# Kernel optimization log

Measured on AMD Instinct MI355X. Metric: run time of the kernel, lower is better.

## Reference

```python
import jax, jax.numpy as jnp
import numpy as np

N = 50000      # nodes
E = 800000     # edges
CIN = 128
CH = 128
COUT = 64
EPS = 1e-5     # BatchNorm eps


def setup_inputs() -> dict:
    key = jax.random.key(0)
    ks = jax.random.split(key, 16)
    s = 0.1  # weight scale for numerical stability
    return {
        "x": jax.random.normal(ks[0], (N, CIN), jnp.float32),
        "edge_index": jax.random.randint(ks[1], (2, E), 0, N, jnp.int32),
        "edge_weights": jax.random.uniform(ks[2], (E,), jnp.float32),
        "w1": jax.random.normal(ks[3], (CIN, CH), jnp.float32) * s,
        "b1": jnp.zeros((CH,), jnp.float32),
        "bn1_g": jnp.ones((CH,), jnp.float32),
        "bn1_b": jnp.zeros((CH,), jnp.float32),
        "bn1_m": jax.random.normal(ks[4], (CH,), jnp.float32) * 0.1,
        "bn1_v": jax.random.uniform(ks[5], (CH,), jnp.float32) + 0.5,
        "conv_ws": jax.random.normal(ks[6], (2, CH, CH), jnp.float32) * s,
        "conv_bs": jnp.zeros((2, CH), jnp.float32),
        "bns_g": jnp.ones((2, CH), jnp.float32),
        "bns_b": jnp.zeros((2, CH), jnp.float32),
        "bns_m": jax.random.normal(ks[7], (2, CH), jnp.float32) * 0.1,
        "bns_v": jax.random.uniform(ks[8], (2, CH), jnp.float32) + 0.5,
        "lin1_w": jax.random.normal(ks[9], (CH, CH), jnp.float32) * s,
        "lin1_b": jnp.zeros((CH,), jnp.float32),
        "lin2_w": jax.random.normal(ks[10], (CH, COUT), jnp.float32) * s,
        "lin2_b": jnp.zeros((COUT,), jnp.float32),
    }


def _bn(h, g, b, m, v):
    # BatchNorm1d in eval mode: running statistics
    return (h - m) * jax.lax.rsqrt(v + EPS) * g + b


def _gcn(h, w, b, src, dst, norm, n):
    # GCNConv: out[dst] += norm_e * (h @ W)[src]  (self loops already in src/dst)
    h = h @ w
    msg = h[src] * norm[:, None]                 # [E+N, CH]
    return jax.ops.segment_sum(msg, dst, num_segments=n) + b


def reference(x, edge_index, edge_weights, w1, b1, bn1_g, bn1_b, bn1_m, bn1_v,
              conv_ws, conv_bs, bns_g, bns_b, bns_m, bns_v,
              lin1_w, lin1_b, lin2_w, lin2_b):
    n = x.shape[0]
    loop = jnp.arange(n, dtype=edge_index.dtype)
    src = jnp.concatenate([edge_index[0], loop])
    dst = jnp.concatenate([edge_index[1], loop])
    ew = jnp.concatenate([edge_weights, jnp.ones((n,), edge_weights.dtype)])
    # symmetric degree normalization (PyG gcn_norm)
    deg = jax.ops.segment_sum(ew, dst, num_segments=n)
    dis = jnp.where(deg > 0, jax.lax.rsqrt(deg), 0.0)
    norm = dis[src] * ew * dis[dst]

    lrelu = jax.nn.leaky_relu  # slope 0.01, matches F.leaky_relu default
    h = lrelu(_bn(_gcn(x, w1, b1, src, dst, norm, n), bn1_g, bn1_b, bn1_m, bn1_v))
    for i in range(conv_ws.shape[0]):
        h = lrelu(_bn(_gcn(h, conv_ws[i], conv_bs[i], src, dst, norm, n),
                      bns_g[i], bns_b[i], bns_m[i], bns_v[i]) + h)
    h = lrelu(h @ lin1_w + lin1_b)
    # dropout is identity in eval mode
    return h @ lin2_w + lin2_b
```

## Files before the change

kernel.cpp:

```cpp
#include <hip/hip_runtime.h>
#include <hip/hip_bf16.h>


constexpr int   NN    = 50000;
constexpr int   EE    = 800000;
constexpr int   CH    = 128;
constexpr int   SLOTS = 64;
constexpr int   NBUK  = 782;
constexpr int   RCAP  = 2048;
constexpr int   EPB   = 4096;
constexpr float EPS   = 1e-5f;

typedef __attribute__((ext_vector_type(8))) short bf16x8;
typedef __attribute__((ext_vector_type(4))) float f32x4;
typedef unsigned long long u64;
typedef unsigned short u16;

__device__ inline u16 f2bf_rne(float f) {
  unsigned u = __float_as_uint(f);
  unsigned r = u + 0x7fffu + ((u >> 16) & 1u);
  return (u16)(r >> 16);
}
__device__ inline float bf2f(unsigned h16) {
  return __uint_as_float(h16 << 16);
}


__global__ __launch_bounds__(256) void bin_kernel(const int* __restrict__ ei,
                                                  const float* __restrict__ ew,
                                                  unsigned* __restrict__ gcur,
                                                  u64* __restrict__ bins) {
  __shared__ unsigned cnt[NBUK];
  __shared__ unsigned base[NBUK];
  const int tid = threadIdx.x;
  for (int b = tid; b < NBUK; b += 256) cnt[b] = 0;
  __syncthreads();
  const int e0 = blockIdx.x * EPB;
  unsigned pk[16]; u16 bkt[16]; u16 rnk[16]; unsigned char dl[16];
  #pragma unroll
  for (int i = 0; i < 16; i++) {
    int e = e0 + i * 256 + tid;
    if (e < EE) {
      int s = ei[e], d = ei[EE + e];
      float w = ew[e];
      bkt[i] = (u16)(d >> 6);
      dl[i]  = (unsigned char)(d & 63);
      pk[i]  = ((unsigned)f2bf_rne(w) << 16) | (unsigned)s;
      rnk[i] = (u16)atomicAdd(&cnt[bkt[i]], 1u);
    } else bkt[i] = 0xffffu;
  }
  __syncthreads();
  for (int b = tid; b < NBUK; b += 256) {
    unsigned c = cnt[b];
    base[b] = c ? atomicAdd(&gcur[b * 16], c) : 0u;
  }
  __syncthreads();
  #pragma unroll
  for (int i = 0; i < 16; i++) {
    if (bkt[i] == 0xffffu) continue;
    unsigned pos = base[bkt[i]] + rnk[i];
    if (pos < RCAP)
      bins[(size_t)bkt[i] * RCAP + pos] = ((u64)dl[i] << 32) | pk[i];
  }
}


__global__ __launch_bounds__(256) void scatter_kernel(const unsigned* __restrict__ gcur,
                                                      const u64* __restrict__ bins,
                                                      unsigned* __restrict__ ell,
                                                      float* __restrict__ dis) {
  __shared__ unsigned rank[64];
  __shared__ float    wsum[64];
  const int b   = blockIdx.x;
  const int tid = threadIdx.x;
  if (tid < 64) { rank[tid] = 1u; wsum[tid] = 0.f; }
  __syncthreads();
  unsigned cnt = gcur[b * 16];
  if (cnt > RCAP) cnt = RCAP;
  const u64* src = bins + (size_t)b * RCAP;
  for (unsigned i = tid; i < cnt; i += 256) {
    u64 v = src[i];
    unsigned pk = (unsigned)v;
    unsigned dl = (unsigned)(v >> 32);
    unsigned r = atomicAdd(&rank[dl], 1u);
    if (r < SLOTS)
      ell[((size_t)(b * 64 + dl)) * SLOTS + r] = pk;
    atomicAdd(&wsum[dl], bf2f(pk >> 16));
  }
  __syncthreads();
  if (tid < 64) {
    int node = b * 64 + tid;
    if (node < NN) {
      unsigned c = rank[tid];
      if (c > SLOTS) c = SLOTS;
      ell[(size_t)node * SLOTS] = c;
      dis[node] = rsqrtf(1.0f + wsum[tid]);
    }
  }
}

constexpr int NB_WZ = (73728 + 384 + 255) / 256;

__global__ void wswz_kernel(
    const float* __restrict__ w1, const float* __restrict__ bn1_g, const float* __restrict__ bn1_v,
    const float* __restrict__ conv_ws, const float* __restrict__ bns_g, const float* __restrict__ bns_v,
    const float* __restrict__ lin1_w, const float* __restrict__ lin2_w,
    const float* __restrict__ b1, const float* __restrict__ bn1_b, const float* __restrict__ bn1_m,
    const float* __restrict__ conv_bs, const float* __restrict__ bns_b, const float* __restrict__ bns_m,
    u16* __restrict__ w1h, u16* __restrict__ w1l,
    u16* __restrict__ c0h, u16* __restrict__ c0l,
    u16* __restrict__ c1h, u16* __restrict__ c1l,
    u16* __restrict__ l1h, u16* __restrict__ l1l,
    u16* __restrict__ l2h, u16* __restrict__ l2l,
    float* __restrict__ beff)
{
  int idx = blockIdx.x * 256 + threadIdx.x;
  if (idx >= 73728) {
    int r = idx - 73728;
    if (r >= 384) return;
    int l = r >> 7, c = r & 127;
    float bc, gg, bb, mm, vv;
    if (l == 0) { bc = b1[c]; gg = bn1_g[c]; bb = bn1_b[c]; mm = bn1_m[c]; vv = bn1_v[c]; }
    else {
      int o = (l - 1) * 128 + c;
      bc = conv_bs[o]; gg = bns_g[o]; bb = bns_b[o]; mm = bns_m[o]; vv = bns_v[o];
    }
    beff[r] = (bc - mm) * gg * rsqrtf(vv + EPS) + bb;
    return;
  }
  const float* W; const float* g = nullptr; const float* v = nullptr;
  u16 *hi, *lo; int CO = 128; int local;
  if      (idx < 16384) { W = w1;              g = bn1_g;     v = bn1_v;     hi = w1h; lo = w1l; local = idx; }
  else if (idx < 32768) { W = conv_ws;         g = bns_g;     v = bns_v;     hi = c0h; lo = c0l; local = idx - 16384; }
  else if (idx < 49152) { W = conv_ws + 16384; g = bns_g+128; v = bns_v+128; hi = c1h; lo = c1l; local = idx - 32768; }
  else if (idx < 65536) { W = lin1_w;                                        hi = l1h; lo = l1l; local = idx - 49152; }
  else                  { W = lin2_w;                                        hi = l2h; lo = l2l; local = idx - 65536; CO = 64; }
  int k = local / CO, n = local % CO;
  float w = W[local];
  if (g) w *= g[n] * rsqrtf(v[n] + EPS);
  int NCT = CO / 16;
  int kchunk = k >> 5, kin = k & 31, quad = kin >> 3, j = kin & 7;
  int ct = n >> 4, l = (quad << 4) | (n & 15);
  size_t pos = ((size_t)(kchunk * NCT + ct) * 64 + l) * 8 + j;
  u16 h = f2bf_rne(w);
  hi[pos] = h;
  lo[pos] = f2bf_rne(w - bf2f(h));
}

__global__ __launch_bounds__(256) void gemm1_kernel(
    const float* __restrict__ Ain,
    const u16* __restrict__ Whi, const u16* __restrict__ Wlo,
    const float* __restrict__ dis, u16* __restrict__ Cout)
{
  __shared__ float lds[64][CH + 4];
  const int tid  = threadIdx.x;
  const int wave = tid >> 6;
  const int lane = tid & 63;
  const int quad = lane >> 4;
  const int mrow = lane & 15;
  const int row0 = blockIdx.x * 64;

  int arow = row0 + wave * 16 + mrow;
  if (arow >= NN) arow = NN - 1;

  bf16x8 ahi[4], alo[4];
  const float* Ar = Ain + (size_t)arow * CH;
  #pragma unroll
  for (int c = 0; c < 4; c++) {
    int off = c * 32 + quad * 8;
    float4 f0 = *(const float4*)(Ar + off);
    float4 f1 = *(const float4*)(Ar + off + 4);
    float f[8] = {f0.x, f0.y, f0.z, f0.w, f1.x, f1.y, f1.z, f1.w};
    #pragma unroll
    for (int j = 0; j < 8; j++) {
      u16 h = f2bf_rne(f[j]);
      ahi[c][j] = (short)h;
      alo[c][j] = (short)f2bf_rne(f[j] - bf2f(h));
    }
  }

  f32x4 acc[8];
  #pragma unroll
  for (int t = 0; t < 8; t++) acc[t] = (f32x4){0.f, 0.f, 0.f, 0.f};
  #pragma unroll
  for (int c = 0; c < 4; c++) {
    #pragma unroll
    for (int t = 0; t < 8; t++) {
      size_t base = ((size_t)(c * 8 + t) * 64 + lane) * 8;
      bf16x8 bh = *(const bf16x8*)(Whi + base);
      bf16x8 bl = *(const bf16x8*)(Wlo + base);
      acc[t] = __builtin_amdgcn_mfma_f32_16x16x32_bf16(ahi[c], bh, acc[t], 0, 0, 0);
      acc[t] = __builtin_amdgcn_mfma_f32_16x16x32_bf16(alo[c], bh, acc[t], 0, 0, 0);
      acc[t] = __builtin_amdgcn_mfma_f32_16x16x32_bf16(ahi[c], bl, acc[t], 0, 0, 0);
    }
  }

  #pragma unroll
  for (int t = 0; t < 8; t++)
    #pragma unroll
    for (int r = 0; r < 4; r++)
      lds[wave * 16 + quad * 4 + r][t * 16 + mrow] = acc[t][r];
  __syncthreads();

  #pragma unroll
  for (int i = tid; i < 64 * CH / 4; i += 256) {
    int row = (i * 4) / CH;
    int col = (i * 4) % CH;
    int grow = row0 + row;
    if (grow >= NN) continue;
    float rs = dis[grow];
    const float* lp = &lds[row][col];
    u16* cp = (u16*)Cout + (size_t)grow * CH + col;
    unsigned p0 = ((unsigned)f2bf_rne(lp[1] * rs) << 16) | f2bf_rne(lp[0] * rs);
    unsigned p1 = ((unsigned)f2bf_rne(lp[3] * rs) << 16) | f2bf_rne(lp[2] * rs);
    *(uint2*)cp = make_uint2(p0, p1);
  }
}

template<bool RES>
__global__ __launch_bounds__(256, 6) void fuse_kernel(
    const u16* __restrict__ hwin,
    const unsigned* __restrict__ ell, const float* __restrict__ dis,
    const float* __restrict__ beff, const u16* __restrict__ res,
    const u16* __restrict__ Whi, const u16* __restrict__ Wlo,
    u16* __restrict__ hout, u16* __restrict__ hwout)
{
  __shared__ unsigned hs[16][68];
  const int tid  = threadIdx.x;
  const int wave = tid >> 6;
  const int lane = tid & 63;
  const int sub  = lane & 15;
  const int grp  = lane >> 4;
  const int row0 = blockIdx.x * 16;

  const int nbase = row0 + wave * 4;
  {
    int nd0 = nbase < NN ? nbase : NN - 1;
    unsigned wcur = ell[(size_t)nd0 * SLOTS + lane];
    for (int r = 0; r < 4; r++) {
      int node = nbase + r;
      int nd = node < NN ? node : NN - 1;
      unsigned myword = wcur;
      if (r < 3) {
        int n2 = node + 1 < NN ? node + 1 : NN - 1;
        wcur = ell[(size_t)n2 * SLOTS + lane];
      }
      int cnt = __shfl((int)myword, 0);
      if (cnt > SLOTS) cnt = SLOTS;
      float a[8] = {0.f, 0.f, 0.f, 0.f, 0.f, 0.f, 0.f, 0.f};
      for (int j = 0; j < cnt; j += 16) {
        unsigned sidx[4]; float wv[4];
        #pragma unroll
        for (int q = 0; q < 4; q++) {
          int jj = j + q * 4 + grp;
          unsigned e = (unsigned)__shfl((int)myword, jj & 63);
          float    w = (jj == 0) ? 1.0f : bf2f(e >> 16);
          unsigned s = (jj == 0) ? (unsigned)nd : (e & 0xffffu);
          if (jj >= cnt) { w = 0.f; s = (unsigned)nd; }
          sidx[q] = s; wv[q] = w;
        }
        uint4 h[4];
        #pragma unroll
        for (int q = 0; q < 4; q++)
          h[q] = *(const uint4*)(hwin + (size_t)sidx[q] * CH + sub * 8);
        #pragma unroll
        for (int q = 0; q < 4; q++) {
          float w = wv[q];
          a[0] = fmaf(w, bf2f(h[q].x & 0xffffu), a[0]); a[1] = fmaf(w, bf2f(h[q].x >> 16), a[1]);
          a[2] = fmaf(w, bf2f(h[q].y & 0xffffu), a[2]); a[3] = fmaf(w, bf2f(h[q].y >> 16), a[3]);
          a[4] = fmaf(w, bf2f(h[q].z & 0xffffu), a[4]); a[5] = fmaf(w, bf2f(h[q].z >> 16), a[5]);
          a[6] = fmaf(w, bf2f(h[q].w & 0xffffu), a[6]); a[7] = fmaf(w, bf2f(h[q].w >> 16), a[7]);
        }
      }
      #pragma unroll
      for (int k = 0; k < 8; k++) {
        a[k] += __shfl_xor(a[k], 16);
        a[k] += __shfl_xor(a[k], 32);
      }
      if (grp == 0) {
        float disd = dis[nd];
        int c = sub * 8;
        float4 be0 = *(const float4*)(beff + c);
        float4 be1 = *(const float4*)(beff + c + 4);
        float y[8];
        y[0] = a[0] * disd + be0.x; y[1] = a[1] * disd + be0.y;
        y[2] = a[2] * disd + be0.z; y[3] = a[3] * disd + be0.w;
        y[4] = a[4] * disd + be1.x; y[5] = a[5] * disd + be1.y;
        y[6] = a[6] * disd + be1.z; y[7] = a[7] * disd + be1.w;
        if constexpr (RES) {
          uint4 rr = *(const uint4*)(res + (size_t)nd * CH + c);
          y[0] += bf2f(rr.x & 0xffffu); y[1] += bf2f(rr.x >> 16);
          y[2] += bf2f(rr.y & 0xffffu); y[3] += bf2f(rr.y >> 16);
          y[4] += bf2f(rr.z & 0xffffu); y[5] += bf2f(rr.z >> 16);
          y[6] += bf2f(rr.w & 0xffffu); y[7] += bf2f(rr.w >> 16);
        }
        #pragma unroll
        for (int k = 0; k < 8; k++) y[k] = y[k] > 0.f ? y[k] : 0.01f * y[k];
        uint4 o;
        o.x = ((unsigned)f2bf_rne(y[1]) << 16) | f2bf_rne(y[0]);
        o.y = ((unsigned)f2bf_rne(y[3]) << 16) | f2bf_rne(y[2]);
        o.z = ((unsigned)f2bf_rne(y[5]) << 16) | f2bf_rne(y[4]);
        o.w = ((unsigned)f2bf_rne(y[7]) << 16) | f2bf_rne(y[6]);
        if (node < NN) *(uint4*)(hout + (size_t)node * CH + c) = o;
        *(uint4*)&hs[wave * 4 + r][sub * 4] = o;
      }
    }
  }
  __syncthreads();

  bf16x8 af[4];
  #pragma unroll
  for (int c = 0; c < 4; c++)
    af[c] = *(const bf16x8*)&hs[sub][c * 16 + grp * 4];

  f32x4 acc[2];
  #pragma unroll
  for (int t = 0; t < 2; t++) acc[t] = (f32x4){0.f, 0.f, 0.f, 0.f};
  #pragma unroll
  for (int c = 0; c < 4; c++) {
    #pragma unroll
    for (int t = 0; t < 2; t++) {
      size_t base = ((size_t)(c * 8 + wave * 2 + t) * 64 + lane) * 8;
      bf16x8 bh = *(const bf16x8*)(Whi + base);
      bf16x8 bl = *(const bf16x8*)(Wlo + base);
      acc[t] = __builtin_amdgcn_mfma_f32_16x16x32_bf16(af[c], bh, acc[t], 0, 0, 0);
      acc[t] = __builtin_amdgcn_mfma_f32_16x16x32_bf16(af[c], bl, acc[t], 0, 0, 0);
    }
  }

  #pragma unroll
  for (int r = 0; r < 4; r++) {
    int grow = row0 + grp * 4 + r;
    if (grow >= NN) continue;
    float rs = dis[grow];
    #pragma unroll
    for (int t = 0; t < 2; t++)
      hwout[(size_t)grow * CH + wave * 32 + t * 16 + sub] = f2bf_rne(acc[t][r] * rs);
  }
}

__global__ __launch_bounds__(256, 6) void fuse_last_kernel(
    const u16* __restrict__ hwin,
    const unsigned* __restrict__ ell, const float* __restrict__ dis,
    const float* __restrict__ beff, const u16* __restrict__ res,
    const u16* __restrict__ l1h, const u16* __restrict__ l1l,
    const float* __restrict__ b1,
    const u16* __restrict__ l2h, const u16* __restrict__ l2l,
    const float* __restrict__ b2, float* __restrict__ out)
{
  __shared__ unsigned hs[16][68];
  __shared__ float    fs[16][132];
  const int tid  = threadIdx.x;
  const int wave = tid >> 6;
  const int lane = tid & 63;
  const int sub  = lane & 15;
  const int grp  = lane >> 4;
  const int row0 = blockIdx.x * 16;

  const int nbase = row0 + wave * 4;
  {
    int nd0 = nbase < NN ? nbase : NN - 1;
    unsigned wcur = ell[(size_t)nd0 * SLOTS + lane];
    for (int r = 0; r < 4; r++) {
      int node = nbase + r;
      int nd = node < NN ? node : NN - 1;
      unsigned myword = wcur;
      if (r < 3) {
        int n2 = node + 1 < NN ? node + 1 : NN - 1;
        wcur = ell[(size_t)n2 * SLOTS + lane];
      }
      int cnt = __shfl((int)myword, 0);
      if (cnt > SLOTS) cnt = SLOTS;
      float a[8] = {0.f, 0.f, 0.f, 0.f, 0.f, 0.f, 0.f, 0.f};
      for (int j = 0; j < cnt; j += 16) {
        unsigned sidx[4]; float wv[4];
        #pragma unroll
        for (int q = 0; q < 4; q++) {
          int jj = j + q * 4 + grp;
          unsigned e = (unsigned)__shfl((int)myword, jj & 63);
          float    w = (jj == 0) ? 1.0f : bf2f(e >> 16);
          unsigned s = (jj == 0) ? (unsigned)nd : (e & 0xffffu);
          if (jj >= cnt) { w = 0.f; s = (unsigned)nd; }
          sidx[q] = s; wv[q] = w;
        }
        uint4 h[4];
        #pragma unroll
        for (int q = 0; q < 4; q++)
          h[q] = *(const uint4*)(hwin + (size_t)sidx[q] * CH + sub * 8);
        #pragma unroll
        for (int q = 0; q < 4; q++) {
          float w = wv[q];
          a[0] = fmaf(w, bf2f(h[q].x & 0xffffu), a[0]); a[1] = fmaf(w, bf2f(h[q].x >> 16), a[1]);
          a[2] = fmaf(w, bf2f(h[q].y & 0xffffu), a[2]); a[3] = fmaf(w, bf2f(h[q].y >> 16), a[3]);
          a[4] = fmaf(w, bf2f(h[q].z & 0xffffu), a[4]); a[5] = fmaf(w, bf2f(h[q].z >> 16), a[5]);
          a[6] = fmaf(w, bf2f(h[q].w & 0xffffu), a[6]); a[7] = fmaf(w, bf2f(h[q].w >> 16), a[7]);
        }
      }
      #pragma unroll
      for (int k = 0; k < 8; k++) {
        a[k] += __shfl_xor(a[k], 16);
        a[k] += __shfl_xor(a[k], 32);
      }
      if (grp == 0) {
        float disd = dis[nd];
        int c = sub * 8;
        float4 be0 = *(const float4*)(beff + c);
        float4 be1 = *(const float4*)(beff + c + 4);
        float y[8];
        y[0] = a[0] * disd + be0.x; y[1] = a[1] * disd + be0.y;
        y[2] = a[2] * disd + be0.z; y[3] = a[3] * disd + be0.w;
        y[4] = a[4] * disd + be1.x; y[5] = a[5] * disd + be1.y;
        y[6] = a[6] * disd + be1.z; y[7] = a[7] * disd + be1.w;
        uint4 rr = *(const uint4*)(res + (size_t)nd * CH + c);
        y[0] += bf2f(rr.x & 0xffffu); y[1] += bf2f(rr.x >> 16);
        y[2] += bf2f(rr.y & 0xffffu); y[3] += bf2f(rr.y >> 16);
        y[4] += bf2f(rr.z & 0xffffu); y[5] += bf2f(rr.z >> 16);
        y[6] += bf2f(rr.w & 0xffffu); y[7] += bf2f(rr.w >> 16);
        #pragma unroll
        for (int k = 0; k < 8; k++) y[k] = y[k] > 0.f ? y[k] : 0.01f * y[k];
        uint4 o;
        o.x = ((unsigned)f2bf_rne(y[1]) << 16) | f2bf_rne(y[0]);
        o.y = ((unsigned)f2bf_rne(y[3]) << 16) | f2bf_rne(y[2]);
        o.z = ((unsigned)f2bf_rne(y[5]) << 16) | f2bf_rne(y[4]);
        o.w = ((unsigned)f2bf_rne(y[7]) << 16) | f2bf_rne(y[6]);
        *(uint4*)&hs[wave * 4 + r][sub * 4] = o;
      }
    }
  }
  __syncthreads();

  bf16x8 af[4];
  #pragma unroll
  for (int c = 0; c < 4; c++)
    af[c] = *(const bf16x8*)&hs[sub][c * 16 + grp * 4];

  f32x4 acc[2];
  #pragma unroll
  for (int t = 0; t < 2; t++) acc[t] = (f32x4){0.f, 0.f, 0.f, 0.f};
  #pragma unroll
  for (int c = 0; c < 4; c++) {
    #pragma unroll
    for (int t = 0; t < 2; t++) {
      size_t base = ((size_t)(c * 8 + wave * 2 + t) * 64 + lane) * 8;
      bf16x8 bh = *(const bf16x8*)(l1h + base);
      bf16x8 bl = *(const bf16x8*)(l1l + base);
      acc[t] = __builtin_amdgcn_mfma_f32_16x16x32_bf16(af[c], bh, acc[t], 0, 0, 0);
      acc[t] = __builtin_amdgcn_mfma_f32_16x16x32_bf16(af[c], bl, acc[t], 0, 0, 0);
    }
  }
  #pragma unroll
  for (int t = 0; t < 2; t++) {
    int col = wave * 32 + t * 16 + sub;
    float bb = b1[col];
    #pragma unroll
    for (int r = 0; r < 4; r++) {
      float x = acc[t][r] + bb;
      x = x > 0.f ? x : 0.01f * x;
      fs[grp * 4 + r][col] = x;
    }
  }
  __syncthreads();

  f32x4 acc2 = (f32x4){0.f, 0.f, 0.f, 0.f};
  #pragma unroll
  for (int c = 0; c < 4; c++) {
    bf16x8 ahi, alo;
    const float* lp = &fs[sub][c * 32 + grp * 8];
    float4 f0 = *(const float4*)lp;
    float4 f1 = *(const float4*)(lp + 4);
    float f[8] = {f0.x, f0.y, f0.z, f0.w, f1.x, f1.y, f1.z, f1.w};
    #pragma unroll
    for (int j = 0; j < 8; j++) {
      u16 h = f2bf_rne(f[j]);
      ahi[j] = (short)h;
      alo[j] = (short)f2bf_rne(f[j] - bf2f(h));
    }
    size_t base = ((size_t)(c * 4 + wave) * 64 + lane) * 8;
    bf16x8 bh = *(const bf16x8*)(l2h + base);
    bf16x8 bl = *(const bf16x8*)(l2l + base);
    acc2 = __builtin_amdgcn_mfma_f32_16x16x32_bf16(ahi, bh, acc2, 0, 0, 0);
    acc2 = __builtin_amdgcn_mfma_f32_16x16x32_bf16(alo, bh, acc2, 0, 0, 0);
    acc2 = __builtin_amdgcn_mfma_f32_16x16x32_bf16(ahi, bl, acc2, 0, 0, 0);
  }
  {
    float bb = b2[wave * 16 + sub];
    #pragma unroll
    for (int r = 0; r < 4; r++) {
      int grow = row0 + grp * 4 + r;
      if (grow < NN)
        out[(size_t)grow * 64 + wave * 16 + sub] = acc2[r] + bb;
    }
  }
}


extern "C" void kernel_launch(void* const* d_in, const int* in_sizes, int n_in,
                              void* d_out, int out_size, void* d_ws, size_t ws_size,
                              hipStream_t stream) {
  const float* x       = (const float*)d_in[0];
  const int*   ei      = (const int*)  d_in[1];
  const float* ew      = (const float*)d_in[2];
  const float* w1      = (const float*)d_in[3];
  const float* b1      = (const float*)d_in[4];
  const float* bn1_g   = (const float*)d_in[5];
  const float* bn1_b   = (const float*)d_in[6];
  const float* bn1_m   = (const float*)d_in[7];
  const float* bn1_v   = (const float*)d_in[8];
  const float* conv_ws = (const float*)d_in[9];
  const float* conv_bs = (const float*)d_in[10];
  const float* bns_g   = (const float*)d_in[11];
  const float* bns_b   = (const float*)d_in[12];
  const float* bns_m   = (const float*)d_in[13];
  const float* bns_v   = (const float*)d_in[14];
  const float* lin1_w  = (const float*)d_in[15];
  const float* lin1_b  = (const float*)d_in[16];
  const float* lin2_w  = (const float*)d_in[17];
  const float* lin2_b  = (const float*)d_in[18];
  float* out = (float*)d_out;

  size_t off = 0;
  auto alloc = [&](size_t elems) -> void* {
    void* p = (char*)d_ws + off * 4;
    off += (elems + 3) & ~(size_t)3;
    return p;
  };
  unsigned* gcur = (unsigned*)alloc(NBUK * 16);
  u64*      bins = (u64*)     alloc((size_t)NBUK * RCAP * 2);
  unsigned* ell  = (unsigned*)alloc((size_t)NN * SLOTS);
  float*    dis  = (float*)   alloc(NN);
  float*    beff = (float*)   alloc(3 * CH);
  u16*      hwa  = (u16*)     alloc((size_t)NN * CH / 2);
  u16*      hwb  = (u16*)     alloc((size_t)NN * CH / 2);
  u16*      h1   = (u16*)     alloc((size_t)NN * CH / 2);
  u16*      h2   = (u16*)     alloc((size_t)NN * CH / 2);
  u16* w1h = (u16*)alloc(CH * CH / 2); u16* w1l = (u16*)alloc(CH * CH / 2);
  u16* c0h = (u16*)alloc(CH * CH / 2); u16* c0l = (u16*)alloc(CH * CH / 2);
  u16* c1h = (u16*)alloc(CH * CH / 2); u16* c1l = (u16*)alloc(CH * CH / 2);
  u16* l1h = (u16*)alloc(CH * CH / 2); u16* l1l = (u16*)alloc(CH * CH / 2);
  u16* l2h = (u16*)alloc(CH * 64 / 2); u16* l2l = (u16*)alloc(CH * 64 / 2);

  const int nb_bin  = (EE + EPB - 1) / EPB;
  const int nb_gemm = (NN + 63) / 64;
  const int nb_fuse = (NN + 15) / 16;
  dim3 B(256);

  hipMemsetAsync(gcur, 0, NBUK * 16 * sizeof(unsigned), stream);
  bin_kernel    <<<nb_bin, B, 0, stream>>>(ei, ew, gcur, bins);
  scatter_kernel<<<NBUK,   B, 0, stream>>>(gcur, bins, ell, dis);

  wswz_kernel<<<NB_WZ, B, 0, stream>>>(w1, bn1_g, bn1_v, conv_ws, bns_g, bns_v,
      lin1_w, lin2_w, b1, bn1_b, bn1_m, conv_bs, bns_b, bns_m,
      w1h, w1l, c0h, c0l, c1h, c1l, l1h, l1l, l2h, l2l, beff);

  gemm1_kernel<<<nb_gemm, B, 0, stream>>>(x, w1h, w1l, dis, hwa);

  fuse_kernel<false><<<nb_fuse, B, 0, stream>>>(hwa, ell, dis, beff, nullptr,
      c0h, c0l, h1, hwb);

  fuse_kernel<true><<<nb_fuse, B, 0, stream>>>(hwb, ell, dis, beff + CH, h1,
      c1h, c1l, h2, hwa);

  fuse_last_kernel<<<nb_fuse, B, 0, stream>>>(hwa, ell, dis, beff + 2 * CH, h2,
      l1h, l1l, lin1_b, l2h, l2l, lin2_b, out);
}
```

Before: 298.5 us.

## Software-pipeline neighbor gathers across nodes and halve edges per bin block

```diff
diff --git a/kernel.cpp b/kernel.cpp
--- a/kernel.cpp
+++ b/kernel.cpp
@@ -8,7 +8,7 @@
 constexpr int   SLOTS = 64;
 constexpr int   NBUK  = 782;
 constexpr int   RCAP  = 2048;
-constexpr int   EPB   = 4096;
+constexpr int   EPB   = 2048;
 constexpr float EPS   = 1e-5f;
 
 typedef __attribute__((ext_vector_type(8))) short bf16x8;
@@ -36,9 +36,9 @@
   for (int b = tid; b < NBUK; b += 256) cnt[b] = 0;
   __syncthreads();
   const int e0 = blockIdx.x * EPB;
-  unsigned pk[16]; u16 bkt[16]; u16 rnk[16]; unsigned char dl[16];
-  #pragma unroll
-  for (int i = 0; i < 16; i++) {
+  unsigned pk[8]; u16 bkt[8]; u16 rnk[8]; unsigned char dl[8];
+  #pragma unroll
+  for (int i = 0; i < 8; i++) {
     int e = e0 + i * 256 + tid;
     if (e < EE) {
       int s = ei[e], d = ei[EE + e];
@@ -56,7 +56,7 @@
   }
   __syncthreads();
   #pragma unroll
-  for (int i = 0; i < 16; i++) {
+  for (int i = 0; i < 8; i++) {
     if (bkt[i] == 0xffffu) continue;
     unsigned pos = base[bkt[i]] + rnk[i];
     if (pos < RCAP)
@@ -217,66 +217,84 @@
   }
 }
 
-template<bool RES>
-__global__ __launch_bounds__(256, 6) void fuse_kernel(
-    const u16* __restrict__ hwin,
-    const unsigned* __restrict__ ell, const float* __restrict__ dis,
-    const float* __restrict__ beff, const u16* __restrict__ res,
-    const u16* __restrict__ Whi, const u16* __restrict__ Wlo,
-    u16* __restrict__ hout, u16* __restrict__ hwout)
+template<bool RES, bool WH>
+__device__ __forceinline__ void gather4_pipe(
+    const u16* __restrict__ hwin, const unsigned* __restrict__ ell,
+    const float* __restrict__ dis, const float* __restrict__ beff,
+    const u16* __restrict__ res, u16* __restrict__ hout,
+    unsigned* __restrict__ hsrow,
+    int nbase, int lane, int sub, int grp)
 {
-  __shared__ unsigned hs[16][68];
-  const int tid  = threadIdx.x;
-  const int wave = tid >> 6;
-  const int lane = tid & 63;
-  const int sub  = lane & 15;
-  const int grp  = lane >> 4;
-  const int row0 = blockIdx.x * 16;
-
-  const int nbase = row0 + wave * 4;
+  auto ndof = [&](int r) { int n = nbase + r; return n < NN ? n : NN - 1; };
+
+  unsigned wcur  = ell[(size_t)ndof(0) * SLOTS + lane];
+  unsigned wnext = ell[(size_t)ndof(1) * SLOTS + lane];
+
+  int r = 0, j = 0;
+  int cnt = __shfl((int)wcur, 0); if (cnt > SLOTS) cnt = SLOTS;
+
+  float a[8] = {0.f, 0.f, 0.f, 0.f, 0.f, 0.f, 0.f, 0.f};
+
+  unsigned sA[4]; float wA[4]; uint4 hA[4];
+
   {
-    int nd0 = nbase < NN ? nbase : NN - 1;
-    unsigned wcur = ell[(size_t)nd0 * SLOTS + lane];
-    for (int r = 0; r < 4; r++) {
-      int node = nbase + r;
-      int nd = node < NN ? node : NN - 1;
-      unsigned myword = wcur;
-      if (r < 3) {
-        int n2 = node + 1 < NN ? node + 1 : NN - 1;
-        wcur = ell[(size_t)n2 * SLOTS + lane];
+    int nd0 = ndof(0);
+    #pragma unroll
+    for (int q = 0; q < 4; q++) {
+      int jj = q * 4 + grp;
+      unsigned e = (unsigned)__shfl((int)wcur, jj);
+      float wv = (jj == 0) ? 1.0f : bf2f(e >> 16);
+      unsigned s = (jj == 0) ? (unsigned)nd0 : (e & 0xffffu);
+      if (jj >= cnt) { wv = 0.f; s = (unsigned)nd0; }
+      sA[q] = s; wA[q] = wv;
+    }
+    #pragma unroll
+    for (int q = 0; q < 4; q++)
+      hA[q] = *(const uint4*)(hwin + (size_t)sA[q] * CH + sub * 8);
+  }
+
+  while (true) {
+    int jn = j + 16, rn = r;
+    const bool cross = (jn >= cnt);
+    if (cross) { rn = r + 1; jn = 0; }
+    const bool havenext = (rn < 4);
+
+    unsigned sB[4]; float wB[4]; uint4 hB[4];
+    int cntN = cnt;
+    if (havenext) {
+      unsigned wsel = cross ? wnext : wcur;
+      if (cross) { cntN = __shfl((int)wnext, 0); if (cntN > SLOTS) cntN = SLOTS; }
+      int ndn = ndof(rn);
+      #pragma unroll
+      for (int q = 0; q < 4; q++) {
+        int jj = jn + q * 4 + grp;
+        unsigned e = (unsigned)__shfl((int)wsel, jj & 63);
+        float wv = (jj == 0) ? 1.0f : bf2f(e >> 16);
+        unsigned s = (jj == 0) ? (unsigned)ndn : (e & 0xffffu);
+        if (jj >= cntN) { wv = 0.f; s = (unsigned)ndn; }
+        sB[q] = s; wB[q] = wv;
       }
-      int cnt = __shfl((int)myword, 0);
-      if (cnt > SLOTS) cnt = SLOTS;
-      float a[8] = {0.f, 0.f, 0.f, 0.f, 0.f, 0.f, 0.f, 0.f};
-      for (int j = 0; j < cnt; j += 16) {
-        unsigned sidx[4]; float wv[4];
-        #pragma unroll
-        for (int q = 0; q < 4; q++) {
-          int jj = j + q * 4 + grp;
-          unsigned e = (unsigned)__shfl((int)myword, jj & 63);
-          float    w = (jj == 0) ? 1.0f : bf2f(e >> 16);
-          unsigned s = (jj == 0) ? (unsigned)nd : (e & 0xffffu);
-          if (jj >= cnt) { w = 0.f; s = (unsigned)nd; }
-          sidx[q] = s; wv[q] = w;
-        }
-        uint4 h[4];
-        #pragma unroll
-        for (int q = 0; q < 4; q++)
-          h[q] = *(const uint4*)(hwin + (size_t)sidx[q] * CH + sub * 8);
-        #pragma unroll
-        for (int q = 0; q < 4; q++) {
-          float w = wv[q];
-          a[0] = fmaf(w, bf2f(h[q].x & 0xffffu), a[0]); a[1] = fmaf(w, bf2f(h[q].x >> 16), a[1]);
-          a[2] = fmaf(w, bf2f(h[q].y & 0xffffu), a[2]); a[3] = fmaf(w, bf2f(h[q].y >> 16), a[3]);
-          a[4] = fmaf(w, bf2f(h[q].z & 0xffffu), a[4]); a[5] = fmaf(w, bf2f(h[q].z >> 16), a[5]);
-          a[6] = fmaf(w, bf2f(h[q].w & 0xffffu), a[6]); a[7] = fmaf(w, bf2f(h[q].w >> 16), a[7]);
-        }
-      }
+      #pragma unroll
+      for (int q = 0; q < 4; q++)
+        hB[q] = *(const uint4*)(hwin + (size_t)sB[q] * CH + sub * 8);
+    }
+
+    #pragma unroll
+    for (int q = 0; q < 4; q++) {
+      float w = wA[q];
+      a[0] = fmaf(w, bf2f(hA[q].x & 0xffffu), a[0]); a[1] = fmaf(w, bf2f(hA[q].x >> 16), a[1]);
+      a[2] = fmaf(w, bf2f(hA[q].y & 0xffffu), a[2]); a[3] = fmaf(w, bf2f(hA[q].y >> 16), a[3]);
+      a[4] = fmaf(w, bf2f(hA[q].z & 0xffffu), a[4]); a[5] = fmaf(w, bf2f(hA[q].z >> 16), a[5]);
+      a[6] = fmaf(w, bf2f(hA[q].w & 0xffffu), a[6]); a[7] = fmaf(w, bf2f(hA[q].w >> 16), a[7]);
+    }
+
+    if (cross) {
       #pragma unroll
       for (int k = 0; k < 8; k++) {
         a[k] += __shfl_xor(a[k], 16);
         a[k] += __shfl_xor(a[k], 32);
       }
+      int nd = ndof(r), node = nbase + r;
       if (grp == 0) {
         float disd = dis[nd];
         int c = sub * 8;
@@ -301,11 +319,43 @@
         o.y = ((unsigned)f2bf_rne(y[3]) << 16) | f2bf_rne(y[2]);
         o.z = ((unsigned)f2bf_rne(y[5]) << 16) | f2bf_rne(y[4]);
         o.w = ((unsigned)f2bf_rne(y[7]) << 16) | f2bf_rne(y[6]);
-        if (node < NN) *(uint4*)(hout + (size_t)node * CH + c) = o;
-        *(uint4*)&hs[wave * 4 + r][sub * 4] = o;
+        if constexpr (WH) {
+          if (node < NN) *(uint4*)(hout + (size_t)node * CH + c) = o;
+        }
+        *(uint4*)&hsrow[r * 68 + sub * 4] = o;
       }
-    }
-  }
+      #pragma unroll
+      for (int k = 0; k < 8; k++) a[k] = 0.f;
+      wcur = wnext;
+      if (r + 2 < 4) wnext = ell[(size_t)ndof(r + 2) * SLOTS + lane];
+      if (havenext) cnt = cntN;
+    }
+
+    if (!havenext) break;
+    r = rn; j = jn;
+    #pragma unroll
+    for (int q = 0; q < 4; q++) { sA[q] = sB[q]; wA[q] = wB[q]; hA[q] = hB[q]; }
+  }
+}
+
+template<bool RES>
+__global__ __launch_bounds__(256, 6) void fuse_kernel(
+    const u16* __restrict__ hwin,
+    const unsigned* __restrict__ ell, const float* __restrict__ dis,
+    const float* __restrict__ beff, const u16* __restrict__ res,
+    const u16* __restrict__ Whi, const u16* __restrict__ Wlo,
+    u16* __restrict__ hout, u16* __restrict__ hwout)
+{
+  __shared__ unsigned hs[16][68];
+  const int tid  = threadIdx.x;
+  const int wave = tid >> 6;
+  const int lane = tid & 63;
+  const int sub  = lane & 15;
+  const int grp  = lane >> 4;
+  const int row0 = blockIdx.x * 16;
+
+  gather4_pipe<RES, true>(hwin, ell, dis, beff, res, hout,
+                          &hs[wave * 4][0], row0 + wave * 4, lane, sub, grp);
   __syncthreads();
 
   bf16x8 af[4];
@@ -357,76 +407,8 @@
   const int grp  = lane >> 4;
   const int row0 = blockIdx.x * 16;
 
-  const int nbase = row0 + wave * 4;
-  {
-    int nd0 = nbase < NN ? nbase : NN - 1;
-    unsigned wcur = ell[(size_t)nd0 * SLOTS + lane];
-    for (int r = 0; r < 4; r++) {
-      int node = nbase + r;
-      int nd = node < NN ? node : NN - 1;
-      unsigned myword = wcur;
-      if (r < 3) {
-        int n2 = node + 1 < NN ? node + 1 : NN - 1;
-        wcur = ell[(size_t)n2 * SLOTS + lane];
-      }
-      int cnt = __shfl((int)myword, 0);
-      if (cnt > SLOTS) cnt = SLOTS;
-      float a[8] = {0.f, 0.f, 0.f, 0.f, 0.f, 0.f, 0.f, 0.f};
-      for (int j = 0; j < cnt; j += 16) {
-        unsigned sidx[4]; float wv[4];
-        #pragma unroll
-        for (int q = 0; q < 4; q++) {
-          int jj = j + q * 4 + grp;
-          unsigned e = (unsigned)__shfl((int)myword, jj & 63);
-          float    w = (jj == 0) ? 1.0f : bf2f(e >> 16);
-          unsigned s = (jj == 0) ? (unsigned)nd : (e & 0xffffu);
-          if (jj >= cnt) { w = 0.f; s = (unsigned)nd; }
-          sidx[q] = s; wv[q] = w;
-        }
-        uint4 h[4];
-        #pragma unroll
-        for (int q = 0; q < 4; q++)
-          h[q] = *(const uint4*)(hwin + (size_t)sidx[q] * CH + sub * 8);
-        #pragma unroll
-        for (int q = 0; q < 4; q++) {
-          float w = wv[q];
-          a[0] = fmaf(w, bf2f(h[q].x & 0xffffu), a[0]); a[1] = fmaf(w, bf2f(h[q].x >> 16), a[1]);
-          a[2] = fmaf(w, bf2f(h[q].y & 0xffffu), a[2]); a[3] = fmaf(w, bf2f(h[q].y >> 16), a[3]);
-          a[4] = fmaf(w, bf2f(h[q].z & 0xffffu), a[4]); a[5] = fmaf(w, bf2f(h[q].z >> 16), a[5]);
-          a[6] = fmaf(w, bf2f(h[q].w & 0xffffu), a[6]); a[7] = fmaf(w, bf2f(h[q].w >> 16), a[7]);
-        }
-      }
-      #pragma unroll
-      for (int k = 0; k < 8; k++) {
-        a[k] += __shfl_xor(a[k], 16);
-        a[k] += __shfl_xor(a[k], 32);
-      }
-      if (grp == 0) {
-        float disd = dis[nd];
-        int c = sub * 8;
-        float4 be0 = *(const float4*)(beff + c);
-        float4 be1 = *(const float4*)(beff + c + 4);
-        float y[8];
-        y[0] = a[0] * disd + be0.x; y[1] = a[1] * disd + be0.y;
-        y[2] = a[2] * disd + be0.z; y[3] = a[3] * disd + be0.w;
-        y[4] = a[4] * disd + be1.x; y[5] = a[5] * disd + be1.y;
-        y[6] = a[6] * disd + be1.z; y[7] = a[7] * disd + be1.w;
-        uint4 rr = *(const uint4*)(res + (size_t)nd * CH + c);
-        y[0] += bf2f(rr.x & 0xffffu); y[1] += bf2f(rr.x >> 16);
-        y[2] += bf2f(rr.y & 0xffffu); y[3] += bf2f(rr.y >> 16);
-        y[4] += bf2f(rr.z & 0xffffu); y[5] += bf2f(rr.z >> 16);
-        y[6] += bf2f(rr.w & 0xffffu); y[7] += bf2f(rr.w >> 16);
-        #pragma unroll
-        for (int k = 0; k < 8; k++) y[k] = y[k] > 0.f ? y[k] : 0.01f * y[k];
-        uint4 o;
-        o.x = ((unsigned)f2bf_rne(y[1]) << 16) | f2bf_rne(y[0]);
-        o.y = ((unsigned)f2bf_rne(y[3]) << 16) | f2bf_rne(y[2]);
-        o.z = ((unsigned)f2bf_rne(y[5]) << 16) | f2bf_rne(y[4]);
-        o.w = ((unsigned)f2bf_rne(y[7]) << 16) | f2bf_rne(y[6]);
-        *(uint4*)&hs[wave * 4 + r][sub * 4] = o;
-      }
-    }
-  }
+  gather4_pipe<true, false>(hwin, ell, dis, beff, res, nullptr,
+                            &hs[wave * 4][0], row0 + wave * 4, lane, sub, grp);
   __syncthreads();
 
   bf16x8 af[4];
```

Result: slower. 368.4 us (+23.4%).
